# Performance work log

Hardware: AMD Instinct MI355X
Metric: run time of the kernel (lower is better)

Reference implementation:

```python
import jax, jax.numpy as jnp
import numpy as np

N_LAYERS = 24  # number of recurrent applications of the shared HashLinear


def setup_inputs() -> dict:
    key = jax.random.key(0)
    ks = jax.random.split(key, 9)
    B, D_IN, N, N_OUT = 1024, 784, 4096, 10
    s_in = 1.0 / np.sqrt(D_IN)
    s_h = 1.0 / np.sqrt(N)
    x = jax.random.normal(ks[0], (B, D_IN), jnp.float32)
    # nn.Linear(prod(input_dim), 2*n_units)
    W_in = jax.random.uniform(ks[1], (2 * N, D_IN), jnp.float32, -s_in, s_in)
    b_in = jax.random.uniform(ks[2], (2 * N,), jnp.float32, -s_in, s_in)
    # HashLinear(n_units, n_units, period=1, 'hash'): learnable +/-1 context key + shared linear
    key_sp = jnp.where(jax.random.bernoulli(ks[3], 0.5, (1, N)), 1.0, -1.0).astype(jnp.float32)
    W_sp = jax.random.uniform(ks[4], (N, N), jnp.float32, -s_h, s_h)
    b_sp = jax.random.uniform(ks[5], (N,), jnp.float32, -s_h, s_h)
    # HashLinear(n_units, 10, period=1, 'hash')
    key_f = jnp.where(jax.random.bernoulli(ks[6], 0.5, (1, N)), 1.0, -1.0).astype(jnp.float32)
    W_f = jax.random.uniform(ks[7], (N_OUT, N), jnp.float32, -s_h, s_h)
    b_f = jax.random.uniform(ks[8], (N_OUT,), jnp.float32, -s_h, s_h)
    return {"x": x, "W_in": W_in, "b_in": b_in, "key_sp": key_sp, "W_sp": W_sp,
            "b_sp": b_sp, "key_f": key_f, "W_f": W_f, "b_f": b_f, "time": 0}


def _hash_linear(xa, xb, o, W, b):
    # Superposition HashLinear: same shared weight applied to both streams,
    # each modulated by the +/-1 context key o ([n_in]).
    ya = (xa * o) @ W.T + b
    yb = (xb * o) @ W.T + b
    return ya, yb


def reference(x, W_in, b_in, key_sp, W_sp, b_sp, key_f, W_f, b_f, time):
    N = W_sp.shape[0]
    r = x @ W_in.T + b_in                 # [B, 2N]
    r_a, r_b = r[:, :N], r[:, N:]         # torch.split(r, n_units, 1)
    pre0 = r_a
    r_a, r_b = jax.nn.relu(r_a), jax.nn.relu(r_b)
    o = key_sp[time % key_sp.shape[0]]    # period=1, time=0 in the module

    def step(carry, _):
        a, b2 = carry
        ya, yb = _hash_linear(a, b2, o, W_sp, b_sp)
        return (jax.nn.relu(ya), jax.nn.relu(yb)), ya  # collect preactivation r_a

    (r_a, r_b), pres = jax.lax.scan(step, (r_a, r_b), None, length=N_LAYERS)
    of = key_f[time % key_f.shape[0]]
    out_a, out_b = _hash_linear(r_a, r_b, of, W_f, b_f)  # [B,10], [B,10]
    preactivations = jnp.concatenate([pre0[None], pres], axis=0)  # [N_LAYERS+1, B, N]
    return (out_a, out_b, preactivations)
```

## Files before the change

kernel.cpp:

```cpp
#include <hip/hip_runtime.h>
#include <hip/hip_bf16.h>
#include <stdint.h>

typedef __bf16 bf16x8 __attribute__((ext_vector_type(8)));
typedef float  f32x4  __attribute__((ext_vector_type(4)));

#define NH      4096
#define MB      1024
#define M2      2048
#define DIN     784
#define KPAD    832
#define N_IN    8192
#define NLAYERS 24
#define NOUT    10

#define ASLOT   (256 * 64)
#define BSLOT   (128 * 64)
#define SLOT    (ASLOT + BSLOT)

__device__ __forceinline__ unsigned short f2bf(float x) {
  union { float f; unsigned u; } v; v.f = x;
  unsigned r = v.u + 0x7FFFu + ((v.u >> 16) & 1u);
  return (unsigned short)(r >> 16);
}
__device__ __forceinline__ float bf2f(unsigned short u) {
  union { unsigned u; float f; } v; v.u = ((unsigned)u) << 16; return v.f;
}

__device__ __forceinline__ void async16(const void* g, void* l) {
  __builtin_amdgcn_global_load_lds(
      (const __attribute__((address_space(1))) void*)g,
      (__attribute__((address_space(3))) void*)l, 16, 0, 0);
}

__global__ void k_conv_wsp(const float* __restrict__ W, const float* __restrict__ o,
                           unsigned short* __restrict__ out) {
  size_t i = ((size_t)blockIdx.x * blockDim.x + threadIdx.x) * 4;
  if (i >= (size_t)NH * NH) return;
  float4 w = *reinterpret_cast<const float4*>(W + i);
  int k = (int)(i & (NH - 1));
  float4 ov = *reinterpret_cast<const float4*>(o + k);
  ushort4 r;
  r.x = f2bf(w.x * ov.x); r.y = f2bf(w.y * ov.y);
  r.z = f2bf(w.z * ov.z); r.w = f2bf(w.w * ov.w);
  *reinterpret_cast<ushort4*>(out + i) = r;
}

__global__ void k_conv_pad(const float* __restrict__ in, unsigned short* __restrict__ out,
                           int rows, int kin, int kout) {
  size_t i = (size_t)blockIdx.x * blockDim.x + threadIdx.x;
  if (i >= (size_t)rows * kout) return;
  int r = (int)(i / kout), c = (int)(i % kout);
  out[i] = (c < kin) ? f2bf(in[(size_t)r * kin + c]) : (unsigned short)0;
}

__device__ __forceinline__ void gemm_core(
    const unsigned short* __restrict__ Ag, const unsigned short* __restrict__ Bg,
    int K, int bm, int bn, unsigned short* lds, f32x4 acc[4][4])
{
  const int t    = threadIdx.x;
  const int lane = t & 63;
  const int wave = t >> 6;
  const int wm   = wave >> 1;
  const int wn   = wave & 1;
  const int l15  = lane & 15;
  const int lkb  = (lane >> 4) * 16;

  const int srow = t >> 3;
  const int sb   = ((t & 7) * 16) ^ ((srow & 7) << 4);
  const unsigned aG0 = (unsigned)((bm + srow) * K + (sb >> 1));
  const unsigned bG0 = (unsigned)((bn + srow) * K + (sb >> 1));

  auto STAGE_P = [&](int slotIdx, int k0, int part) {
    unsigned short* s = lds + slotIdx * SLOT;
    const int ja = part * 2;
    async16(Ag + aG0 + (unsigned)((ja + 0) * 64 * K + k0), s + t * 8 + (ja + 0) * 4096);
    async16(Ag + aG0 + (unsigned)((ja + 1) * 64 * K + k0), s + t * 8 + (ja + 1) * 4096);
    async16(Bg + bG0 + (unsigned)(part * 64 * K + k0), s + ASLOT + t * 8 + part * 4096);
  };

  int aRd[2][4], bRd[2][4];
#pragma unroll
  for (int kk = 0; kk < 2; ++kk)
#pragma unroll
    for (int i = 0; i < 4; ++i) {
      const int ra = wm * 64 + i * 16 + l15;
      aRd[kk][i] = (ra * 128 + ((kk * 64 + lkb) ^ ((ra & 7) << 4))) >> 1;
      const int rb = wn * 64 + i * 16 + l15;
      bRd[kk][i] = (rb * 128 + ((kk * 64 + lkb) ^ ((rb & 7) << 4))) >> 1;
    }

  const int nt = K >> 6;
  STAGE_P(0, 0, 0);  STAGE_P(0, 0, 1);
  STAGE_P(1, 64, 0); STAGE_P(1, 64, 1);
  asm volatile("s_waitcnt vmcnt(6)" ::: "memory");
  __builtin_amdgcn_s_barrier();

  int s0 = 0, s2 = 2;
  for (int kt = 0; kt < nt; ++kt) {
    const unsigned short* base = lds + s0 * SLOT;
#pragma unroll
    for (int half = 0; half < 2; ++half) {
      bf16x8 A4[4], B4[4];
#pragma unroll
      for (int i = 0; i < 4; ++i) A4[i] = *reinterpret_cast<const bf16x8*>(base + aRd[half][i]);
#pragma unroll
      for (int i = 0; i < 4; ++i) B4[i] = *reinterpret_cast<const bf16x8*>(base + ASLOT + bRd[half][i]);
      if (kt + 2 < nt) STAGE_P(s2, (kt + 2) << 6, half);
      if (half == 1) {
        if (kt + 2 < nt)      asm volatile("s_waitcnt vmcnt(6)" ::: "memory");
        else if (kt + 1 < nt) asm volatile("s_waitcnt vmcnt(0)" ::: "memory");
      }
      __builtin_amdgcn_s_barrier();
      asm volatile("s_waitcnt lgkmcnt(0)" ::: "memory");
      __builtin_amdgcn_sched_barrier(0);
      __builtin_amdgcn_s_setprio(1);
#pragma unroll
      for (int mi = 0; mi < 4; ++mi)
#pragma unroll
        for (int ni = 0; ni < 4; ++ni)
          acc[mi][ni] = __builtin_amdgcn_mfma_f32_16x16x32_bf16(A4[mi], B4[ni], acc[mi][ni], 0, 0, 0);
      __builtin_amdgcn_s_setprio(0);
      __builtin_amdgcn_s_barrier();
    }
    const int ns0 = (s0 == 2) ? 0 : s0 + 1;
    const int ns2 = (s2 == 2) ? 0 : s2 + 1;
    s0 = ns0; s2 = ns2;
  }
}

__global__ __launch_bounds__(512, 2) void k_gemm_layer(
    const unsigned short* __restrict__ A, const unsigned short* __restrict__ W,
    const float* __restrict__ bias, float* __restrict__ preact,
    unsigned short* __restrict__ Anext)
{
  __shared__ __align__(16) unsigned short lds[3 * SLOT];
  const int bid = blockIdx.x;
  const int s   = ((bid & 7) << 5) + (bid >> 3);
  const int bm = (s >> 5) * 256;
  const int bn = (s & 31) * 128;
  f32x4 acc[4][4] = {};
  gemm_core(A, W, NH, bm, bn, lds, acc);

  const int lane = threadIdx.x & 63;
  const int wave = threadIdx.x >> 6;
  const int wm = (wave >> 1) * 64, wn = (wave & 1) * 64;
  const int l15 = lane & 15;
#pragma unroll
  for (int mi = 0; mi < 4; ++mi) {
    const int gm0 = bm + wm + mi * 16 + (lane >> 4) * 4;
#pragma unroll
    for (int ni = 0; ni < 4; ++ni) {
      const int gn = bn + wn + ni * 16 + l15;
      const float bv = bias[gn];
#pragma unroll
      for (int r = 0; r < 4; ++r) {
        const int gm = gm0 + r;
        const float y = acc[mi][ni][r] + bv;
        if (gm < MB) preact[(size_t)gm * NH + gn] = y;
        Anext[(size_t)gm * NH + gn] = f2bf(y > 0.f ? y : 0.f);
      }
    }
  }
}

__global__ __launch_bounds__(512, 2) void k_gemm_in(
    const unsigned short* __restrict__ X, const unsigned short* __restrict__ W,
    const float* __restrict__ bias, float* __restrict__ preact0,
    unsigned short* __restrict__ A0)
{
  __shared__ __align__(16) unsigned short lds[3 * SLOT];
  const int bid = blockIdx.x;
  const int s   = ((bid & 7) << 5) + (bid >> 3);
  const int bm = (s >> 6) * 256;
  const int bn = (s & 63) * 128;
  f32x4 acc[4][4] = {};
  gemm_core(X, W, KPAD, bm, bn, lds, acc);

  const int lane = threadIdx.x & 63;
  const int wave = threadIdx.x >> 6;
  const int wm = (wave >> 1) * 64, wn = (wave & 1) * 64;
  const int l15 = lane & 15;
#pragma unroll
  for (int mi = 0; mi < 4; ++mi) {
    const int gm0 = bm + wm + mi * 16 + (lane >> 4) * 4;
#pragma unroll
    for (int ni = 0; ni < 4; ++ni) {
      const int gn = bn + wn + ni * 16 + l15;
      const float bv = bias[gn];
#pragma unroll
      for (int r = 0; r < 4; ++r) {
        const int gm = gm0 + r;
        const float y = acc[mi][ni][r] + bv;
        const unsigned short rl = f2bf(y > 0.f ? y : 0.f);
        if (gn < NH) {
          preact0[(size_t)gm * NH + gn] = y;
          A0[(size_t)gm * NH + gn] = rl;
        } else {
          A0[(size_t)(MB + gm) * NH + (gn - NH)] = rl;
        }
      }
    }
  }
}

__global__ void k_final(const unsigned short* __restrict__ A,
                        const float* __restrict__ Wf, const float* __restrict__ of,
                        const float* __restrict__ bf_, float* __restrict__ out)
{
  const int m = blockIdx.x;
  const int t = threadIdx.x;
  float accj[NOUT] = {};
  for (int k = t; k < NH; k += 256) {
    const float a = bf2f(A[(size_t)m * NH + k]) * of[k];
#pragma unroll
    for (int j = 0; j < NOUT; ++j) accj[j] += a * Wf[j * NH + k];
  }
  __shared__ float red[4][NOUT];
#pragma unroll
  for (int j = 0; j < NOUT; ++j) {
    float v = accj[j];
    for (int off = 32; off > 0; off >>= 1) v += __shfl_down(v, off);
    if ((t & 63) == 0) red[t >> 6][j] = v;
  }
  __syncthreads();
  if (t < NOUT) {
    const float s = red[0][t] + red[1][t] + red[2][t] + red[3][t] + bf_[t];
    out[(size_t)m * NOUT + t] = s;
  }
}

extern "C" void kernel_launch(void* const* d_in, const int* in_sizes, int n_in,
                              void* d_out, int out_size, void* d_ws, size_t ws_size,
                              hipStream_t stream) {
  const float* x     = (const float*)d_in[0];
  const float* W_in  = (const float*)d_in[1];
  const float* b_in  = (const float*)d_in[2];
  const float* keysp = (const float*)d_in[3];
  const float* W_sp  = (const float*)d_in[4];
  const float* b_sp  = (const float*)d_in[5];
  const float* keyf  = (const float*)d_in[6];
  const float* W_f   = (const float*)d_in[7];
  const float* b_f   = (const float*)d_in[8];

  float* out    = (float*)d_out;
  float* preact = out + (size_t)2 * MB * NOUT;

  char* ws = (char*)d_ws;
  unsigned short* Wsp_bf = (unsigned short*)ws;  ws += (size_t)NH * NH * 2;
  unsigned short* A0     = (unsigned short*)ws;  ws += (size_t)M2 * NH * 2;
  unsigned short* A1     = (unsigned short*)ws;  ws += (size_t)M2 * NH * 2;
  unsigned short* Win_bf = (unsigned short*)ws;  ws += (size_t)N_IN * KPAD * 2;
  unsigned short* X_bf   = (unsigned short*)ws;  ws += (size_t)MB * KPAD * 2;

  k_conv_wsp<<<(NH * (size_t)NH / 4 + 255) / 256, 256, 0, stream>>>(W_sp, keysp, Wsp_bf);
  k_conv_pad<<<((size_t)N_IN * KPAD + 255) / 256, 256, 0, stream>>>(W_in, Win_bf, N_IN, DIN, KPAD);
  k_conv_pad<<<((size_t)MB * KPAD + 255) / 256, 256, 0, stream>>>(x, X_bf, MB, DIN, KPAD);

  k_gemm_in<<<256, 512, 0, stream>>>(X_bf, Win_bf, b_in, preact, A0);

  unsigned short* Ain = A0;
  unsigned short* Aout = A1;
  for (int tlay = 0; tlay < NLAYERS; ++tlay) {
    float* pre = preact + (size_t)(tlay + 1) * MB * NH;
    k_gemm_layer<<<256, 512, 0, stream>>>(Ain, Wsp_bf, b_sp, pre, Aout);
    unsigned short* tmp = Ain; Ain = Aout; Aout = tmp;
  }

  k_final<<<M2, 256, 0, stream>>>(Ain, W_f, keyf, b_f, out);
}
```

Before: 1.739 ms.

## Shrink GEMM tiles to 128x128 with 256 threads and double buffering

The GEMM core moves from a 256x128 tile with 512 threads and a triple-buffered, half-step staging scheme to a 128x128 tile with 256 threads and a simple double buffer. It prefetches the next K tile before computing the current one. The launch grid doubles to 512 blocks, and a new XCD-aware block mapping groups N columns per XCD. The aim is more blocks per GPU and lower LDS use, at the cost of less data reuse per tile and a simpler pipeline that waits on vmcnt(0) every step.

```diff
diff --git a/kernel.cpp b/kernel.cpp
--- a/kernel.cpp
+++ b/kernel.cpp
@@ -14,9 +14,8 @@
 #define NLAYERS 24
 #define NOUT    10
 
-#define ASLOT   (256 * 64)
-#define BSLOT   (128 * 64)
-#define SLOT    (ASLOT + BSLOT)
+#define ASL     (128 * 64)
+#define SLOT    (2 * ASL)
 
 __device__ __forceinline__ unsigned short f2bf(float x) {
   union { float f; unsigned u; } v; v.f = x;
@@ -71,12 +70,14 @@
   const unsigned aG0 = (unsigned)((bm + srow) * K + (sb >> 1));
   const unsigned bG0 = (unsigned)((bn + srow) * K + (sb >> 1));
 
-  auto STAGE_P = [&](int slotIdx, int k0, int part) {
-    unsigned short* s = lds + slotIdx * SLOT;
-    const int ja = part * 2;
-    async16(Ag + aG0 + (unsigned)((ja + 0) * 64 * K + k0), s + t * 8 + (ja + 0) * 4096);
-    async16(Ag + aG0 + (unsigned)((ja + 1) * 64 * K + k0), s + t * 8 + (ja + 1) * 4096);
-    async16(Bg + bG0 + (unsigned)(part * 64 * K + k0), s + ASLOT + t * 8 + part * 4096);
+  auto STAGE = [&](int bufIdx, int k0) {
+    unsigned short* s = lds + bufIdx * SLOT;
+#pragma unroll
+    for (int j = 0; j < 4; ++j)
+      async16(Ag + aG0 + (unsigned)(j * 32 * K + k0), s + t * 8 + j * 2048);
+#pragma unroll
+    for (int j = 0; j < 4; ++j)
+      async16(Bg + bG0 + (unsigned)(j * 32 * K + k0), s + ASL + t * 8 + j * 2048);
   };
 
   int aRd[2][4], bRd[2][4];
@@ -91,54 +92,48 @@
     }
 
   const int nt = K >> 6;
-  STAGE_P(0, 0, 0);  STAGE_P(0, 0, 1);
-  STAGE_P(1, 64, 0); STAGE_P(1, 64, 1);
-  asm volatile("s_waitcnt vmcnt(6)" ::: "memory");
+  STAGE(0, 0);
+  asm volatile("s_waitcnt vmcnt(0)" ::: "memory");
   __builtin_amdgcn_s_barrier();
 
-  int s0 = 0, s2 = 2;
+  int buf = 0;
   for (int kt = 0; kt < nt; ++kt) {
-    const unsigned short* base = lds + s0 * SLOT;
-#pragma unroll
-    for (int half = 0; half < 2; ++half) {
-      bf16x8 A4[4], B4[4];
-#pragma unroll
-      for (int i = 0; i < 4; ++i) A4[i] = *reinterpret_cast<const bf16x8*>(base + aRd[half][i]);
-#pragma unroll
-      for (int i = 0; i < 4; ++i) B4[i] = *reinterpret_cast<const bf16x8*>(base + ASLOT + bRd[half][i]);
-      if (kt + 2 < nt) STAGE_P(s2, (kt + 2) << 6, half);
-      if (half == 1) {
-        if (kt + 2 < nt)      asm volatile("s_waitcnt vmcnt(6)" ::: "memory");
-        else if (kt + 1 < nt) asm volatile("s_waitcnt vmcnt(0)" ::: "memory");
-      }
+    if (kt + 1 < nt) STAGE(buf ^ 1, (kt + 1) << 6);
+    const unsigned short* base = lds + buf * SLOT;
+    __builtin_amdgcn_s_setprio(1);
+#pragma unroll
+    for (int kk = 0; kk < 2; ++kk) {
+      bf16x8 a[4], b[4];
+#pragma unroll
+      for (int i = 0; i < 4; ++i) a[i] = *reinterpret_cast<const bf16x8*>(base + aRd[kk][i]);
+#pragma unroll
+      for (int i = 0; i < 4; ++i) b[i] = *reinterpret_cast<const bf16x8*>(base + ASL + bRd[kk][i]);
+#pragma unroll
+      for (int mi = 0; mi < 4; ++mi)
+#pragma unroll
+        for (int ni = 0; ni < 4; ++ni)
+          acc[mi][ni] = __builtin_amdgcn_mfma_f32_16x16x32_bf16(a[mi], b[ni], acc[mi][ni], 0, 0, 0);
+    }
+    __builtin_amdgcn_s_setprio(0);
+    if (kt + 1 < nt) {
+      asm volatile("s_waitcnt vmcnt(0)" ::: "memory");
       __builtin_amdgcn_s_barrier();
-      asm volatile("s_waitcnt lgkmcnt(0)" ::: "memory");
-      __builtin_amdgcn_sched_barrier(0);
-      __builtin_amdgcn_s_setprio(1);
-#pragma unroll
-      for (int mi = 0; mi < 4; ++mi)
-#pragma unroll
-        for (int ni = 0; ni < 4; ++ni)
-          acc[mi][ni] = __builtin_amdgcn_mfma_f32_16x16x32_bf16(A4[mi], B4[ni], acc[mi][ni], 0, 0, 0);
-      __builtin_amdgcn_s_setprio(0);
-      __builtin_amdgcn_s_barrier();
-    }
-    const int ns0 = (s0 == 2) ? 0 : s0 + 1;
-    const int ns2 = (s2 == 2) ? 0 : s2 + 1;
-    s0 = ns0; s2 = ns2;
-  }
-}
-
-__global__ __launch_bounds__(512, 2) void k_gemm_layer(
+    }
+    buf ^= 1;
+  }
+}
+
+__global__ __launch_bounds__(256, 2) void k_gemm_layer(
     const unsigned short* __restrict__ A, const unsigned short* __restrict__ W,
     const float* __restrict__ bias, float* __restrict__ preact,
     unsigned short* __restrict__ Anext)
 {
-  __shared__ __align__(16) unsigned short lds[3 * SLOT];
+  __shared__ __align__(16) unsigned short lds[2 * SLOT];
   const int bid = blockIdx.x;
-  const int s   = ((bid & 7) << 5) + (bid >> 3);
-  const int bm = (s >> 5) * 256;
-  const int bn = (s & 31) * 128;
+  const int xcd = bid & 7;
+  const int idx = bid >> 3;
+  const int bm  = (idx >> 2) * 128;
+  const int bn  = (xcd * 4 + (idx & 3)) * 128;
   f32x4 acc[4][4] = {};
   gemm_core(A, W, NH, bm, bn, lds, acc);
 
@@ -164,16 +159,17 @@
   }
 }
 
-__global__ __launch_bounds__(512, 2) void k_gemm_in(
+__global__ __launch_bounds__(256, 2) void k_gemm_in(
     const unsigned short* __restrict__ X, const unsigned short* __restrict__ W,
     const float* __restrict__ bias, float* __restrict__ preact0,
     unsigned short* __restrict__ A0)
 {
-  __shared__ __align__(16) unsigned short lds[3 * SLOT];
+  __shared__ __align__(16) unsigned short lds[2 * SLOT];
   const int bid = blockIdx.x;
-  const int s   = ((bid & 7) << 5) + (bid >> 3);
-  const int bm = (s >> 6) * 256;
-  const int bn = (s & 63) * 128;
+  const int xcd = bid & 7;
+  const int idx = bid >> 3;
+  const int bm  = (idx >> 3) * 128;
+  const int bn  = (xcd * 8 + (idx & 7)) * 128;
   f32x4 acc[4][4] = {};
   gemm_core(X, W, KPAD, bm, bn, lds, acc);
 
@@ -257,13 +253,13 @@
   k_conv_pad<<<((size_t)N_IN * KPAD + 255) / 256, 256, 0, stream>>>(W_in, Win_bf, N_IN, DIN, KPAD);
   k_conv_pad<<<((size_t)MB * KPAD + 255) / 256, 256, 0, stream>>>(x, X_bf, MB, DIN, KPAD);
 
-  k_gemm_in<<<256, 512, 0, stream>>>(X_bf, Win_bf, b_in, preact, A0);
+  k_gemm_in<<<512, 256, 0, stream>>>(X_bf, Win_bf, b_in, preact, A0);
 
   unsigned short* Ain = A0;
   unsigned short* Aout = A1;
   for (int tlay = 0; tlay < NLAYERS; ++tlay) {
     float* pre = preact + (size_t)(tlay + 1) * MB * NH;
-    k_gemm_layer<<<256, 512, 0, stream>>>(Ain, Wsp_bf, b_sp, pre, Aout);
+    k_gemm_layer<<<512, 256, 0, stream>>>(Ain, Wsp_bf, b_sp, pre, Aout);
     unsigned short* tmp = Ain; Ain = Aout; Aout = tmp;
   }
 
```

Result: faster. 1.610 ms (-7.4%).
